# Kernel optimization log

Measured on AMD Instinct MI355X. Metric: run time of the kernel, lower is better.

## Reference

```python
import jax, jax.numpy as jnp
import numpy as np

DIM = 64   # model dim == d_inner (expand=1)
Hh = 64
Ww = 64
BATCH = 4
D_IN = 64
N_ST = 8   # d_state
DT_R = 4   # dt_rank = ceil(dim/16)
K = 4      # depthwise conv kernel
NB = 8     # total CrossMambaBlocks: 4 (depth=1) + 4 final cross blocks


def setup_inputs():
    key = jax.random.key(0)
    ks = iter(jax.random.split(key, 40))
    def rn(shape, s=0.02):
        return jax.random.normal(next(ks), shape, jnp.float32) * s
    A_init = jnp.log(jnp.tile(jnp.arange(1, N_ST + 1, dtype=jnp.float32), (NB, D_IN, 1)))
    return dict(
        img1=rn((BATCH, DIM, Hh, Ww), 1.0), img2=rn((BATCH, DIM, Hh, Ww), 1.0),
        img1_sum=rn((BATCH, DIM, Hh, Ww), 1.0), img2_sum=rn((BATCH, DIM, Hh, Ww), 1.0),
        norm0_w=jnp.ones((NB, DIM)), norm0_b=jnp.zeros((NB, DIM)),
        norm1_w=jnp.ones((NB, DIM)), norm1_b=jnp.zeros((NB, DIM)),
        in_w=rn((NB, 2 * D_IN, DIM)), in_b=jnp.zeros((NB, 2 * D_IN)),
        conv_w_f=rn((NB, D_IN, 1, K), 0.1), conv_b_f=jnp.zeros((NB, D_IN)),
        conv_w_b=rn((NB, D_IN, 1, K), 0.1), conv_b_b=jnp.zeros((NB, D_IN)),
        xproj_w_f=rn((NB, DT_R + 2 * N_ST, D_IN)), xproj_w_b=rn((NB, DT_R + 2 * N_ST, D_IN)),
        dtproj_w_f=rn((NB, D_IN, DT_R), 0.1), dtproj_b_f=jnp.zeros((NB, D_IN)),
        dtproj_w_b=rn((NB, D_IN, DT_R), 0.1), dtproj_b_b=jnp.zeros((NB, D_IN)),
        A_log_f=A_init, A_log_b=A_init,
        D_f=jnp.ones((NB, D_IN)), D_b=jnp.ones((NB, D_IN)),
        ln_w=jnp.ones((NB, D_IN)), ln_b=jnp.zeros((NB, D_IN)),
        mout_w=rn((NB, DIM, D_IN)), mout_b=jnp.zeros((NB, DIM)),
        fop_w=rn((DIM, 2 * DIM)), fop_b=jnp.zeros((DIM,)),
    )


def _ln(x, w, b):
    m = x.mean(-1, keepdims=True)
    v = ((x - m) ** 2).mean(-1, keepdims=True)
    return (x - m) * jax.lax.rsqrt(v + 1e-5) * w + b


def _dwconv(x, w, b):
    # x: [b,L,d], w: [d,1,K] depthwise causal conv along L
    y = jax.lax.conv_general_dilated(
        x.transpose(0, 2, 1), w, (1,), [(K - 1, 0)],
        dimension_numbers=('NCH', 'OIH', 'NCH'),
        feature_group_count=x.shape[-1])
    return y.transpose(0, 2, 1) + b


def _ssm(u, dt, Bm, Cm, A, Dm):
    # u,dt: [b,L,d]; Bm,Cm: [b,L,n]; A: [d,n]; Dm: [d]
    dA = jnp.exp(dt[..., None] * A)                 # [b,L,d,n]
    dBu = (dt * u)[..., None] * Bm[:, :, None, :]   # [b,L,d,n]
    def step(h, xs):
        dA_t, dBu_t, C_t = xs
        h = dA_t * h + dBu_t
        return h, jnp.einsum('bdn,bn->bd', h, C_t)
    h0 = jnp.zeros(u.shape[:1] + A.shape, u.dtype)
    _, ys = jax.lax.scan(step, h0, (jnp.moveaxis(dA, 1, 0), jnp.moveaxis(dBu, 1, 0), jnp.moveaxis(Cm, 1, 0)))
    return jnp.moveaxis(ys, 0, 1) + u * Dm


def _direction(x_in, extra, conv_w, conv_b, xproj_w, dtproj_w, dtproj_b, A_log, Dm, flip):
    if flip:
        x_in = x_in[:, ::-1]
        extra = extra[:, ::-1]
    u = jax.nn.silu(_dwconv(x_in, conv_w, conv_b))
    dbl = jnp.einsum('bld,ed->ble', extra, xproj_w)     # cross: dt/B/C from extra embedding
    dtr = dbl[..., :DT_R]
    Bm = dbl[..., DT_R:DT_R + N_ST]
    Cm = dbl[..., DT_R + N_ST:]
    dt = jax.nn.softplus(jnp.einsum('blr,dr->bld', dtr, dtproj_w) + dtproj_b)
    y = _ssm(u, dt, Bm, Cm, -jnp.exp(A_log), Dm)
    if flip:
        y = y[:, ::-1]
    return y


def _cross_block(i, x, extra, p):
    skip = x
    x = _ln(x, p['norm0_w'][i], p['norm0_b'][i])
    extra = _ln(extra, p['norm1_w'][i], p['norm1_b'][i])
    xz = jnp.einsum('bld,ed->ble', x, p['in_w'][i]) + p['in_b'][i]
    x_in, z = xz[..., :D_IN], xz[..., D_IN:]
    y_f = _direction(x_in, extra, p['conv_w_f'][i], p['conv_b_f'][i], p['xproj_w_f'][i],
                     p['dtproj_w_f'][i], p['dtproj_b_f'][i], p['A_log_f'][i], p['D_f'][i], False)
    y_b = _direction(x_in, extra, p['conv_w_b'][i], p['conv_b_b'][i], p['xproj_w_b'][i],
                     p['dtproj_w_b'][i], p['dtproj_b_b'][i], p['A_log_b'][i], p['D_b'][i], True)
    y = 0.5 * (y_f + y_b)                    # if_devide_out=True
    y = _ln(y, p['ln_w'][i], p['ln_b'][i])   # use_norm=True
    y = y * jax.nn.silu(z)
    out = jnp.einsum('bld,ed->ble', y, p['mout_w'][i]) + p['mout_b'][i]
    return out + skip


def _forward(img1, img2, img1_sum, img2_sum, norm0_w, norm0_b, norm1_w, norm1_b, in_w, in_b,
             conv_w_f, conv_b_f, conv_w_b, conv_b_b, xproj_w_f, xproj_w_b,
             dtproj_w_f, dtproj_b_f, dtproj_w_b, dtproj_b_b, A_log_f, A_log_b,
             D_f, D_b, ln_w, ln_b, mout_w, mout_b, fop_w, fop_b):
    p = dict(norm0_w=norm0_w, norm0_b=norm0_b, norm1_w=norm1_w, norm1_b=norm1_b,
             in_w=in_w, in_b=in_b, conv_w_f=conv_w_f, conv_b_f=conv_b_f,
             conv_w_b=conv_w_b, conv_b_b=conv_b_b, xproj_w_f=xproj_w_f, xproj_w_b=xproj_w_b,
             dtproj_w_f=dtproj_w_f, dtproj_b_f=dtproj_b_f, dtproj_w_b=dtproj_w_b,
             dtproj_b_b=dtproj_b_b, A_log_f=A_log_f, A_log_b=A_log_b, D_f=D_f, D_b=D_b,
             ln_w=ln_w, ln_b=ln_b, mout_w=mout_w, mout_b=mout_b)
    def seq(t):
        b, c, h, w = t.shape
        return t.reshape(b, c, h * w).transpose(0, 2, 1)   # b (h w) c
    s1, s2, s1s, s2s = seq(img1), seq(img2), seq(img1_sum), seq(img2_sum)
    # depth=1 cross-fusion loop
    s1 = _cross_block(0, s1, s1s, p)
    s2 = _cross_block(1, s2, s2s, p)
    s1s = _cross_block(2, s1s, s1, p)
    s2s = _cross_block(3, s2s, s2, p)
    # final cross blocks
    i1l = _cross_block(4, s1, s2, p)
    i1g = _cross_block(5, s1, s2s, p)
    i2l = _cross_block(6, s2, s1, p)
    i2g = _cross_block(7, s2, s1s, p)
    c1 = jnp.concatenate([i1l, i1g], -1)
    c2 = jnp.concatenate([i2l, i2g], -1)
    fusion = jnp.einsum('ble,ce->blc', 0.5 * (c1 + c2), fop_w) + fop_b
    b = img1.shape[0]
    return fusion.transpose(0, 2, 1).reshape(b, DIM, Hh, Ww)


def reference(img1, img2, img1_sum, img2_sum, norm0_w, norm0_b, norm1_w, norm1_b, in_w, in_b,
              conv_w_f, conv_b_f, conv_w_b, conv_b_b, xproj_w_f, xproj_w_b,
              dtproj_w_f, dtproj_b_f, dtproj_w_b, dtproj_b_b, A_log_f, A_log_b,
              D_f, D_b, ln_w, ln_b, mout_w, mout_b, fop_w, fop_b):
    return _forward(img1, img2, img1_sum, img2_sum, norm0_w, norm0_b, norm1_w, norm1_b, in_w, in_b,
                    conv_w_f, conv_b_f, conv_w_b, conv_b_b, xproj_w_f, xproj_w_b,
                    dtproj_w_f, dtproj_b_f, dtproj_w_b, dtproj_b_b, A_log_f, A_log_b,
                    D_f, D_b, ln_w, ln_b, mout_w, mout_b, fop_w, fop_b)
```

## Files before the change

### kernel.cpp

```cpp
#include <hip/hip_runtime.h>
#include <hip/hip_bf16.h>

#define BX 4
#define LX 4096
#define DX 64
#define NX 8
#define TCH 16
#define NCH 256
#define BLD (BX*LX*DX)

typedef unsigned short u16;
typedef __attribute__((ext_vector_type(8))) short v8s;
typedef __attribute__((ext_vector_type(4))) float v4f;

#define L2E 1.44269504088896f
#define LN2 0.69314718055994531f

__device__ __forceinline__ float b2f(u16 u){ return __uint_as_float(((unsigned)u)<<16); }
__device__ __forceinline__ u16 f2b(float f){
  unsigned u = __float_as_uint(f);
  unsigned r = (u + 0x7FFFu + ((u>>16)&1u)) >> 16;
  return (u16)r;
}
__device__ __forceinline__ float siluf(float x){
  return x * __builtin_amdgcn_rcpf(1.f + __builtin_amdgcn_exp2f(-x*L2E));
}
__device__ __forceinline__ float softplusf(float x){
  const float t = __builtin_amdgcn_exp2f(-fabsf(x)*L2E);
  return fmaxf(x, 0.f) + LN2 * __builtin_amdgcn_logf(1.f + t);
}

__device__ __forceinline__ v4f mfma16(v8s a, v8s b, v4f c){
  return __builtin_amdgcn_mfma_f32_16x16x32_bf16(a, b, c, 0, 0, 0);
}
__device__ __forceinline__ void split8(const float* v, v8s& hi, v8s& lo){
  #pragma unroll
  for(int j=0;j<8;j++){
    const short h = (short)f2b(v[j]);
    hi[j] = h;
    lo[j] = (short)f2b(v[j] - b2f((u16)h));
  }
}
__device__ __forceinline__ void afrag(const float* tile, int lane, int k0, v8s& hi, v8s& lo){
  const float* p = tile + (lane&15)*72 + k0 + ((lane>>4)<<3);
  float v[8];
  const float4 a = *(const float4*)(p);
  const float4 b = *(const float4*)(p+4);
  v[0]=a.x; v[1]=a.y; v[2]=a.z; v[3]=a.w;
  v[4]=b.x; v[5]=b.y; v[6]=b.z; v[7]=b.w;
  split8(v, hi, lo);
}

struct Ctx {
  const float *nw0,*nb0,*nw1,*nb1;
  const float *inb;
  const float *convw,*convb;
  const float *dtw,*dtb;
  const float *A2,*Dp;
  const float *lnw,*lnb;
  const float *moutb;
  const float *fopb;
  const u16 *wih,*wil,*wxh,*wxl,*wmh,*wml,*wfh,*wfl;
  float *act[4], *outc[4];
  float *xin[4], *zz[4], *dbl[4], *yy[4], *Pp[4], *qq[4], *hin[4];
};

struct BlkDesc { int i; const float* x; const float* e; float* out; int slot; };
struct StageArgs { BlkDesc d[4]; };

struct PrepEnt { const void* src; float* dst; int n; int mode; };
struct PrepAll { PrepEnt a[21]; };
struct WPrep { const void* sA; const void* sB; u16* dh; u16* dl; long off; int E; int KS; int kind; int i; };
struct WPrepAll { WPrep a[25]; };

__global__ __launch_bounds__(256) void k_prep(PrepAll pa, WPrepAll wa, const u16* df){
  const bool isbf = (df[0] == 0x3F80u);
  if(blockIdx.y < 21){
    PrepEnt p = pa.a[blockIdx.y];
    int idx = blockIdx.x*256 + threadIdx.x;
    if(idx < p.n){
      float v = isbf ? b2f(((const u16*)p.src)[idx]) : ((const float*)p.src)[idx];
      if(p.mode==2) v = -__expf(v) * L2E;
      p.dst[idx] = v;
    }
  } else {
    WPrep p = wa.a[blockIdx.y - 21];
    const int wv = threadIdx.x >> 6, lane = threadIdx.x & 63;
    const int idx = blockIdx.x*4 + wv;
    const int NT = (p.E + 15) >> 4;
    if(idx >= NT*p.KS) return;
    const int ct = idx / p.KS, ks = idx % p.KS;
    const int g  = ct*16 + (lane & 15);
    const int k0 = ks*32 + ((lane>>4)<<3);
    const int K  = p.KS*32;
    bool valid; long si = 0; const void* sp = p.sA;
    if(p.kind == 1){
      valid = (g < 40);
      const int dir = g/20, e = g - dir*20;
      if(dir) sp = p.sB;
      si = ((long)p.i*20 + e)*64 + k0;
    } else {
      valid = (g < p.E);
      si = p.off + (long)g*K + k0;
    }
    float v[8];
    #pragma unroll
    for(int j2=0;j2<8;j2++){
      float x = 0.f;
      if(valid) x = isbf ? b2f(((const u16*)sp)[si+j2]) : ((const float*)sp)[si+j2];
      v[j2] = x;
    }
    v8s hi, lo; split8(v, hi, lo);
    const size_t o = ((size_t)idx*64 + lane)*8;
    *(v8s*)(p.dh + o) = hi;
    *(v8s*)(p.dl + o) = lo;
  }
}

struct SeqArgs { const void* src[4]; };

__global__ __launch_bounds__(256) void k_seq(SeqArgs s, Ctx c, const u16* df){
  const bool isbf = (df[0] == 0x3F80u);
  __shared__ float ld[64*65];
  const int t = blockIdx.z, b = blockIdx.y, l0 = blockIdx.x*64;
  float* dst = c.act[t];
  const int tx = threadIdx.x, ty = threadIdx.y;
  if(isbf){
    const u16* src = (const u16*)s.src[t];
    #pragma unroll
    for(int k=0;k<16;k++){ int d = k*4+ty; ld[d*65+tx] = b2f(src[(size_t)(b*64+d)*LX + l0+tx]); }
  } else {
    const float* src = (const float*)s.src[t];
    #pragma unroll
    for(int k=0;k<16;k++){ int d = k*4+ty; ld[d*65+tx] = src[(size_t)(b*64+d)*LX + l0+tx]; }
  }
  __syncthreads();
  #pragma unroll
  for(int k=0;k<16;k++){ int p = k*4+ty; dst[(size_t)(b*LX + l0+p)*64 + tx] = ld[tx*65+p]; }
}

__device__ __forceinline__ void coop72(float* sb, const float* g, int t){
  #pragma unroll
  for(int k=0;k<4;k++){
    const int idx = k*256 + t;
    const int row = idx >> 4;
    const int c4  = (idx & 15) << 2;
    *(float4*)(sb + row*72 + c4) = *(const float4*)(g + (size_t)row*64 + c4);
  }
}
__device__ __forceinline__ void coop72_avg(float* sb, const float* g0, const float* g1, int t){
  #pragma unroll
  for(int k=0;k<4;k++){
    const int idx = k*256 + t;
    const int row = idx >> 4;
    const int c4  = (idx & 15) << 2;
    const float4 a = *(const float4*)(g0 + (size_t)row*64 + c4);
    const float4 b = *(const float4*)(g1 + (size_t)row*64 + c4);
    float4 o; o.x=0.5f*(a.x+b.x); o.y=0.5f*(a.y+b.y); o.z=0.5f*(a.z+b.z); o.w=0.5f*(a.w+b.w);
    *(float4*)(sb + row*72 + c4) = o;
  }
}

__device__ __forceinline__ void ln72(float* sb, int lane, const float* w, const float* b){
  float r[64];
  float* p = sb + lane*72;
  #pragma unroll
  for(int cc=0;cc<64;cc+=4){ float4 v = *(const float4*)(p+cc); r[cc]=v.x; r[cc+1]=v.y; r[cc+2]=v.z; r[cc+3]=v.w; }
  float m=0.f;
  #pragma unroll
  for(int d=0;d<64;d++) m += r[d];
  m *= (1.f/64.f);
  float va=0.f;
  #pragma unroll
  for(int d=0;d<64;d++){ float t=r[d]-m; va += t*t; }
  va *= (1.f/64.f);
  const float rs = rsqrtf(va + 1e-5f);
  #pragma unroll
  for(int d=0;d<64;d++) r[d] = (r[d]-m)*rs*w[d] + b[d];
  #pragma unroll
  for(int cc=0;cc<64;cc+=4){ float4 v={r[cc],r[cc+1],r[cc+2],r[cc+3]}; *(float4*)(p+cc)=v; }
}

__global__ __launch_bounds__(256) void k_front(Ctx c, StageArgs sa){
  __shared__ __align__(16) float sx[64*72];
  __shared__ __align__(16) float se[64*72];
  const BlkDesc bd = sa.d[blockIdx.y];
  const int i = bd.i;
  const int tile = blockIdx.x;
  const int b = tile >> 6;
  const int l0 = (tile & 63) << 6;
  const int bl0 = b*LX + l0;
  const int t = threadIdx.x;
  const int wave = t >> 6, lane = t & 63;

  coop72(sx, bd.x + (size_t)bl0*64, t);
  coop72(se, bd.e + (size_t)bl0*64, t);
  __syncthreads();
  if(wave == 0)      ln72(sx, lane, c.nw0 + i*64, c.nb0 + i*64);
  else if(wave == 1) ln72(se, lane, c.nw1 + i*64, c.nb1 + i*64);
  __syncthreads();

  const int m0 = wave*16;
  const int q  = lane >> 4;
  const int n15 = lane & 15;

  {
    v8s ah[2], al[2];
    afrag(sx + m0*72, lane, 0,  ah[0], al[0]);
    afrag(sx + m0*72, lane, 32, ah[1], al[1]);
    const v8s* WH = (const v8s*)c.wih + (size_t)i*1024;
    const v8s* WL = (const v8s*)c.wil + (size_t)i*1024;
    #pragma unroll 1
    for(int ct=0; ct<8; ct++){
      const int colg = ct*16 + n15;
      const float bias = c.inb[i*128 + colg];
      v4f acc = {bias, bias, bias, bias};
      #pragma unroll
      for(int ks=0; ks<2; ks++){
        const v8s wh = WH[(ct*2+ks)*64 + lane];
        const v8s wl = WL[(ct*2+ks)*64 + lane];
        acc = mfma16(ah[ks], wl, acc);
        acc = mfma16(al[ks], wh, acc);
        acc = mfma16(ah[ks], wh, acc);
      }
      float* baseo = (colg < 64) ? c.xin[bd.slot] : c.zz[bd.slot];
      const int col = colg & 63;
      #pragma unroll
      for(int r=0;r<4;r++){
        const int row = m0 + q*4 + r;
        baseo[(size_t)(bl0+row)*64 + col] = acc[r];
      }
    }
  }
  {
    v8s ah[2], al[2];
    afrag(se + m0*72, lane, 0,  ah[0], al[0]);
    afrag(se + m0*72, lane, 32, ah[1], al[1]);
    const v8s* WH = (const v8s*)c.wxh + (size_t)i*384;
    const v8s* WL = (const v8s*)c.wxl + (size_t)i*384;
    #pragma unroll 1
    for(int ct=0; ct<3; ct++){
      v4f acc = {0.f,0.f,0.f,0.f};
      #pragma unroll
      for(int ks=0; ks<2; ks++){
        const v8s wh = WH[(ct*2+ks)*64 + lane];
        const v8s wl = WL[(ct*2+ks)*64 + lane];
        acc = mfma16(ah[ks], wl, acc);
        acc = mfma16(al[ks], wh, acc);
        acc = mfma16(ah[ks], wh, acc);
      }
      const int g = ct*16 + n15;
      if(g < 40){
        const int dir = (g >= 20);
        const int e = g - dir*20;
        float* dp = c.dbl[bd.slot] + (size_t)dir*((size_t)BX*LX*20);
        #pragma unroll
        for(int r=0;r<4;r++){
          const int row = m0 + q*4 + r;
          dp[(size_t)(bl0+row)*20 + e] = acc[r];
        }
      }
    }
  }
}

template<int PASS>
__device__ __forceinline__ void scan_body(const Ctx& c, const StageArgs& sa){
  __shared__ __align__(16) float meta[TCH*20];
  const int zid = blockIdx.z;
  const int j = zid >> 1, dir = zid & 1;
  const BlkDesc bd = sa.d[j];
  const int i = bd.i, slot = bd.slot;
  const int ch = blockIdx.x, b = blockIdx.y;
  const int d = threadIdx.x;
  const int pb = (dir*8 + i)*64 + d;

  const float4 cwv = *(const float4*)(c.convw + (size_t)pb*4);
  const float  cbv = c.convb[pb];
  const float4 dwv = *(const float4*)(c.dtw + (size_t)pb*4);
  const float  dtbv = c.dtb[pb];
  const float4 A2a = *(const float4*)(c.A2 + (size_t)pb*8);
  const float4 A2b = *(const float4*)(c.A2 + (size_t)pb*8 + 4);
  float A2[8] = {A2a.x,A2a.y,A2a.z,A2a.w,A2b.x,A2b.y,A2b.z,A2b.w};

  {
    const float4* s = (const float4*)(c.dbl[slot] + (size_t)dir*((size_t)BX*LX*20)
                                      + (size_t)(b*LX + ch*TCH)*20);
    float4* dst = (float4*)meta;
    #pragma unroll
    for(int k=0;k<2;k++){ int idx = k*64 + d; if(idx < 80) dst[idx] = s[idx]; }
  }
  __syncthreads();

  const float* X = c.xin[slot] + (size_t)b*LX*64 + d;
  float h[8];
  if(PASS==1){
    #pragma unroll
    for(int n=0;n<8;n++) h[n]=0.f;
  } else {
    const float* hp = c.hin[slot] + (size_t)(dir*NCH + ch)*((size_t)BX*512) + (size_t)b*512 + d;
    #pragma unroll
    for(int n=0;n<8;n++) h[n] = hp[n*64];
  }
  const float Dv = (PASS==3) ? c.Dp[pb] : 0.f;
  float* Y = (PASS==3) ? (c.yy[slot] + (size_t)(dir*BX + b)*LX*64 + d) : (float*)0;

  int lbase, sgn;
  if(dir==0){ lbase = ch*TCH;          sgn =  1; }
  else      { lbase = ch*TCH + TCH-1;  sgn = -1; }
  float w0,w1,w2;
  { int p0 = lbase - 3*sgn; w0 = (p0>=0 && p0<LX)? X[(size_t)p0*64] : 0.f; }
  { int p1 = lbase - 2*sgn; w1 = (p1>=0 && p1<LX)? X[(size_t)p1*64] : 0.f; }
  { int p2 = lbase - 1*sgn; w2 = (p2>=0 && p2<LX)? X[(size_t)p2*64] : 0.f; }

  const float* Xp = X + (size_t)lbase*64;
  float* Yp = (PASS==3) ? (Y + (size_t)lbase*64) : (float*)0;
  const float* mp = meta + (dir ? (TCH-1)*20 : 0);
  const int xstep = sgn*64;
  const int mstep = sgn*20;

  float S = 0.f;
  #pragma unroll 4
  for(int t=0;t<TCH;t++){
    const float xc = *Xp;
    const float u = siluf(cwv.x*w0 + cwv.y*w1 + cwv.z*w2 + cwv.w*xc + cbv);
    const float4 m0  = *(const float4*)(mp);
    const float4 mb0 = *(const float4*)(mp+4);
    const float4 mb1 = *(const float4*)(mp+8);
    const float dt = softplusf(m0.x*dwv.x + m0.y*dwv.y + m0.z*dwv.z + m0.w*dwv.w + dtbv);
    const float du = dt*u;
    const float Bv[8] = {mb0.x,mb0.y,mb0.z,mb0.w,mb1.x,mb1.y,mb1.z,mb1.w};
    #pragma unroll
    for(int n=0;n<8;n++){
      const float dA = __builtin_amdgcn_exp2f(dt*A2[n]);
      h[n] = dA*h[n] + du*Bv[n];
    }
    if(PASS==3){
      const float4 mc0 = *(const float4*)(mp+12);
      const float4 mc1 = *(const float4*)(mp+16);
      const float Cv[8] = {mc0.x,mc0.y,mc0.z,mc0.w,mc1.x,mc1.y,mc1.z,mc1.w};
      float yv = u*Dv;
      #pragma unroll
      for(int n=0;n<8;n++) yv += h[n]*Cv[n];
      *Yp = yv;
      Yp += xstep;
    } else {
      S += dt;
    }
    w0=w1; w1=w2; w2=xc;
    Xp += xstep; mp += mstep;
  }
  if(PASS==1){
    float* Pw = c.Pp[slot] + (size_t)(dir*NCH + ch)*((size_t)BX*512) + (size_t)b*512 + d;
    float* Qw = c.qq[slot] + (size_t)(dir*NCH + ch)*((size_t)BX*512) + (size_t)b*512 + d;
    #pragma unroll
    for(int n=0;n<8;n++){
      Pw[n*64] = __builtin_amdgcn_exp2f(A2[n]*S);
      Qw[n*64] = h[n];
    }
  }
}

__global__ __launch_bounds__(64) void k_scan1(Ctx c, StageArgs sa){ scan_body<1>(c, sa); }
__global__ __launch_bounds__(64) void k_scan3(Ctx c, StageArgs sa){ scan_body<3>(c, sa); }

__global__ __launch_bounds__(64) void k_mid(Ctx c, StageArgs sa){
  const int b = blockIdx.x >> 3;
  const int seg = blockIdx.x & 7;
  const int dir = blockIdx.y & 1, j = blockIdx.y >> 1;
  const BlkDesc bd = sa.d[j];
  const int slot = bd.slot;
  const int nd = seg*64 + threadIdx.x;
  const size_t base = (size_t)dir*NCH*((size_t)BX*512) + (size_t)b*512 + nd;
  const size_t STR = (size_t)BX*512;
  const float* P = c.Pp[slot] + base;
  const float* Q = c.qq[slot] + base;
  float* H = c.hin[slot] + base;
  float h = 0.f;
  float Pv[32], Qv[32];
  #pragma unroll 1
  for(int g=0; g<NCH/32; g++){
    #pragma unroll
    for(int k=0;k<32;k++){
      const int ch = dir ? (NCH-1 - (g*32+k)) : (g*32+k);
      Pv[k] = P[(size_t)ch*STR]; Qv[k] = Q[(size_t)ch*STR];
    }
    #pragma unroll
    for(int k=0;k<32;k++){
      const int ch = dir ? (NCH-1 - (g*32+k)) : (g*32+k);
      H[(size_t)ch*STR] = h;
      h = fmaf(Pv[k], h, Qv[k]);
    }
  }
}

__global__ __launch_bounds__(256) void k_back(Ctx c, StageArgs sa){
  __shared__ __align__(16) float sy[64*72];
  __shared__ __align__(16) float sz[64*72];
  __shared__ __align__(16) float sk[64*72];
  const BlkDesc bd = sa.d[blockIdx.y];
  const int i = bd.i, slot = bd.slot;
  const int tile = blockIdx.x;
  const int b = tile >> 6;
  const int l0 = (tile & 63) << 6;
  const int bl0 = b*LX + l0;
  const int t = threadIdx.x;
  const int wave = t >> 6, lane = t & 63;

  coop72_avg(sy, c.yy[slot] + (size_t)b*LX*64 + (size_t)l0*64,
                 c.yy[slot] + (size_t)(BX+b)*LX*64 + (size_t)l0*64, t);
  coop72(sz, c.zz[slot] + (size_t)bl0*64, t);
  coop72(sk, bd.x + (size_t)bl0*64, t);
  __syncthreads();
  if(wave == 0){
    ln72(sy, lane, c.lnw + i*64, c.lnb + i*64);
    float* p = sy + lane*72;
    const float* zp = sz + lane*72;
    #pragma unroll
    for(int d=0;d<64;d++){ p[d] *= siluf(zp[d]); }
  }
  __syncthreads();

  const int m0 = wave*16;
  const int q  = lane >> 4;
  const int n15 = lane & 15;
  v8s ah[2], al[2];
  afrag(sy + m0*72, lane, 0,  ah[0], al[0]);
  afrag(sy + m0*72, lane, 32, ah[1], al[1]);
  const v8s* WH = (const v8s*)c.wmh + (size_t)i*512;
  const v8s* WL = (const v8s*)c.wml + (size_t)i*512;
  #pragma unroll 1
  for(int ct=0; ct<4; ct++){
    const int col = ct*16 + n15;
    const float bias = c.moutb[i*64 + col];
    v4f acc = {bias, bias, bias, bias};
    #pragma unroll
    for(int ks=0; ks<2; ks++){
      const v8s wh = WH[(ct*2+ks)*64 + lane];
      const v8s wl = WL[(ct*2+ks)*64 + lane];
      acc = mfma16(ah[ks], wl, acc);
      acc = mfma16(al[ks], wh, acc);
      acc = mfma16(ah[ks], wh, acc);
    }
    #pragma unroll
    for(int r=0;r<4;r++){
      const int row = m0 + q*4 + r;
      bd.out[(size_t)(bl0+row)*64 + col] = acc[r] + sk[row*72 + col];
    }
  }
}

__global__ __launch_bounds__(256) void k_fusion(Ctx c, void* outp, const u16* df){
  const bool isbf = (df[0] == 0x3F80u);
  __shared__ __align__(16) float sL[64*72];
  __shared__ __align__(16) float sH[64*72];
  __shared__ __align__(16) float sT[64*68];
  const int tile = blockIdx.x;
  const int b = tile >> 6;
  const int l0 = (tile & 63) << 6;
  const int bl0 = b*LX + l0;
  const int t = threadIdx.x;
  const int wave = t >> 6, lane = t & 63;

  coop72_avg(sL, c.outc[0] + (size_t)bl0*64, c.outc[2] + (size_t)bl0*64, t);
  coop72_avg(sH, c.outc[1] + (size_t)bl0*64, c.outc[3] + (size_t)bl0*64, t);
  __syncthreads();

  const int m0 = wave*16;
  const int q  = lane >> 4;
  const int n15 = lane & 15;
  v8s ah[4], al[4];
  afrag(sL + m0*72, lane, 0,  ah[0], al[0]);
  afrag(sL + m0*72, lane, 32, ah[1], al[1]);
  afrag(sH + m0*72, lane, 0,  ah[2], al[2]);
  afrag(sH + m0*72, lane, 32, ah[3], al[3]);
  const v8s* WH = (const v8s*)c.wfh;
  const v8s* WL = (const v8s*)c.wfl;
  #pragma unroll 1
  for(int ct=0; ct<4; ct++){
    const int col = ct*16 + n15;
    const float bias = c.fopb[col];
    v4f acc = {bias, bias, bias, bias};
    #pragma unroll
    for(int ks=0; ks<4; ks++){
      const v8s wh = WH[(ct*4+ks)*64 + lane];
      const v8s wl = WL[(ct*4+ks)*64 + lane];
      acc = mfma16(ah[ks], wl, acc);
      acc = mfma16(al[ks], wh, acc);
      acc = mfma16(ah[ks], wh, acc);
    }
    #pragma unroll
    for(int r=0;r<4;r++) sT[col*68 + m0 + q*4 + r] = acc[r];
  }
  __syncthreads();

  const int o  = t >> 2;
  const int p0 = (t & 3) * 16;
  float v[16];
  #pragma unroll
  for(int k=0;k<16;k+=4){
    const float4 x = *(const float4*)(sT + o*68 + p0 + k);
    v[k]=x.x; v[k+1]=x.y; v[k+2]=x.z; v[k+3]=x.w;
  }
  const size_t off = (size_t)(b*64+o)*LX + l0 + p0;
  if(isbf){
    u16 hb[16];
    #pragma unroll
    for(int k=0;k<16;k++) hb[k] = f2b(v[k]);
    uint4 u0, u1;
    u0.x = hb[0] | ((unsigned)hb[1]<<16);  u0.y = hb[2] | ((unsigned)hb[3]<<16);
    u0.z = hb[4] | ((unsigned)hb[5]<<16);  u0.w = hb[6] | ((unsigned)hb[7]<<16);
    u1.x = hb[8] | ((unsigned)hb[9]<<16);  u1.y = hb[10]| ((unsigned)hb[11]<<16);
    u1.z = hb[12]| ((unsigned)hb[13]<<16); u1.w = hb[14]| ((unsigned)hb[15]<<16);
    *(uint4*)((u16*)outp + off)     = u0;
    *(uint4*)((u16*)outp + off + 8) = u1;
  } else {
    float* fo = (float*)outp + off;
    #pragma unroll
    for(int k=0;k<16;k+=4){ float4 x={v[k],v[k+1],v[k+2],v[k+3]}; *(float4*)(fo+k)=x; }
  }
}

extern "C" void kernel_launch(void* const* d_in, const int* in_sizes, int n_in,
                              void* d_out, int out_size, void* d_ws, size_t ws_size,
                              hipStream_t stream){
  (void)in_sizes; (void)out_size;
  if(n_in < 30) return;
  const u16* df = (const u16*)d_in[22];
  float* w = (float*)d_ws;
  size_t off = 0;
  auto al = [&](size_t n){ float* p = w + off; off += n; return p; };

  Ctx c;
  float* nw0 = al(512);  float* nb0 = al(512);
  float* nw1 = al(512);  float* nb1 = al(512);
  float* inb = al(1024);
  float* convw = al(4096); float* convb = al(1024);
  float* dtw = al(4096); float* dtb = al(1024);
  float* A2 = al(8192);  float* Dp = al(1024);
  float* lnw = al(512);  float* lnb = al(512);
  float* moutb = al(512);
  float* fopb = al(64);
  c.nw0=nw0; c.nb0=nb0; c.nw1=nw1; c.nb1=nb1;
  c.inb=inb; c.convw=convw; c.convb=convb;
  c.dtw=dtw; c.dtb=dtb; c.A2=A2; c.Dp=Dp;
  c.lnw=lnw; c.lnb=lnb; c.moutb=moutb; c.fopb=fopb;

  u16* wih = (u16*)al(32768); u16* wil = (u16*)al(32768);
  u16* wxh = (u16*)al(12288); u16* wxl = (u16*)al(12288);
  u16* wmh = (u16*)al(16384); u16* wml = (u16*)al(16384);
  u16* wfh = (u16*)al(4096);  u16* wfl = (u16*)al(4096);
  c.wih=wih; c.wil=wil; c.wxh=wxh; c.wxl=wxl; c.wmh=wmh; c.wml=wml; c.wfh=wfh; c.wfl=wfl;

  for(int k=0;k<4;k++) c.act[k]  = al(BLD);
  for(int k=0;k<4;k++) c.outc[k] = al(BLD);

  const size_t CHW = 2*(size_t)NCH*BX*512;
  const size_t SLOT = (size_t)BLD + BLD + 2*(size_t)BX*LX*20 + 2*(size_t)BLD + 3*CHW;
  const size_t avail = ws_size/4;
  int nslots = 4;
  while(nslots>1 && off + (size_t)nslots*SLOT > avail) nslots >>= 1;
  for(int s=0;s<nslots;s++){
    c.xin[s]=al(BLD); c.zz[s]=al(BLD); c.dbl[s]=al(2*(size_t)BX*LX*20);
    c.yy[s]=al(2*(size_t)BLD);
    c.Pp[s]=al(CHW); c.qq[s]=al(CHW); c.hin[s]=al(CHW);
  }
  for(int s=nslots;s<4;s++){
    c.xin[s]=c.xin[0]; c.zz[s]=c.zz[0]; c.dbl[s]=c.dbl[0]; c.yy[s]=c.yy[0];
    c.Pp[s]=c.Pp[0]; c.qq[s]=c.qq[0]; c.hin[s]=c.hin[0];
  }

  PrepAll pa;
  int kk = 0;
  auto add = [&](int idx, float* dst, int n, int mode){
    pa.a[kk].src=d_in[idx]; pa.a[kk].dst=dst; pa.a[kk].n=n; pa.a[kk].mode=mode; kk++;
  };
  add(4,  nw0, 512, 0); add(5,  nb0, 512, 0);
  add(6,  nw1, 512, 0); add(7,  nb1, 512, 0);
  add(9,  inb, 1024, 0);
  add(10, convw, 2048, 0);      add(11, convb, 512, 0);
  add(12, convw+2048, 2048, 0); add(13, convb+512, 512, 0);
  add(16, dtw, 2048, 0);        add(17, dtb, 512, 0);
  add(18, dtw+2048, 2048, 0);   add(19, dtb+512, 512, 0);
  add(20, A2, 4096, 2);         add(21, A2+4096, 4096, 2);
  add(22, Dp, 512, 0);          add(23, Dp+512, 512, 0);
  add(24, lnw, 512, 0);         add(25, lnb, 512, 0);
  add(27, moutb, 512, 0);
  add(29, fopb, 64, 0);

  WPrepAll wa;
  for(int i=0;i<8;i++) wa.a[i]    = { d_in[8],  nullptr,  wih+(size_t)i*8192, wil+(size_t)i*8192, (long)i*8192, 128, 2, 0, i };
  for(int i=0;i<8;i++) wa.a[8+i]  = { d_in[14], d_in[15], wxh+(size_t)i*3072, wxl+(size_t)i*3072, 0,            48, 2, 1, i };
  for(int i=0;i<8;i++) wa.a[16+i] = { d_in[26], nullptr,  wmh+(size_t)i*4096, wml+(size_t)i*4096, (long)i*4096, 64, 2, 0, i };
  wa.a[24] = { d_in[28], nullptr, wfh, wfl, 0, 64, 4, 0, 0 };

  k_prep<<<dim3(16,46),256,0,stream>>>(pa, wa, df);

  SeqArgs sq;
  for(int t=0;t<4;t++) sq.src[t] = d_in[t];
  k_seq<<<dim3(64,BX,4), dim3(64,4), 0, stream>>>(sq, c, df);

  BlkDesc R1[2] = {{0, c.act[0], c.act[2], c.act[0], 0},
                   {1, c.act[1], c.act[3], c.act[1], 0}};
  BlkDesc R2[4] = {{2, c.act[2], c.act[0], c.act[2], 0},
                   {3, c.act[3], c.act[1], c.act[3], 0},
                   {4, c.act[0], c.act[1], c.outc[0], 0},
                   {6, c.act[1], c.act[0], c.outc[2], 0}};
  BlkDesc R3[2] = {{5, c.act[0], c.act[3], c.outc[1], 0},
                   {7, c.act[1], c.act[2], c.outc[3], 0}};

  auto run = [&](BlkDesc* ds, int cnt){
    for(int k=0;k<cnt;k+=nslots){
      int n = cnt-k; if(n>nslots) n = nslots;
      StageArgs sa;
      for(int j=0;j<n;j++){ sa.d[j] = ds[k+j]; sa.d[j].slot = j; }
      for(int j=n;j<4;j++) sa.d[j] = sa.d[0];
      k_front<<<dim3(256,n),      256, 0, stream>>>(c, sa);
      k_scan1<<<dim3(NCH,BX,2*n),  64, 0, stream>>>(c, sa);
      k_mid  <<<dim3(BX*8,2*n),    64, 0, stream>>>(c, sa);
      k_scan3<<<dim3(NCH,BX,2*n),  64, 0, stream>>>(c, sa);
      k_back <<<dim3(256,n),      256, 0, stream>>>(c, sa);
    }
  };
  run(R1,2); run(R2,4); run(R3,2);
  k_fusion<<<256,256,0,stream>>>(c, d_out, df);
}
```

Baseline: 376.5 us.

## Fuse chunk scan passes into front and back kernels, drop yy buffer

Folds the first scan pass (chunk-local state and decay products) into k_front. It reuses the in-projection outputs and x_proj metadata already held in shared memory, and recomputes a 3-row conv halo on each side of the tile with a scalar LN plus projection. The second scan pass moves into k_back, which averages both directions straight into shared memory. That removes the yy global buffer and two kernel launches per stage. The cost is redundant halo recomputation, more register pressure from the 22-element x windows and unrolled loops, and fewer waves running scans than the separate kernels had.

```diff
diff --git a/kernel.cpp b/kernel.cpp
--- a/kernel.cpp
+++ b/kernel.cpp
@@ -60,31 +60,40 @@
   const float *lnw,*lnb;
   const float *moutb;
   const float *fopb;
+  const float *inwxT;
   const u16 *wih,*wil,*wxh,*wxl,*wmh,*wml,*wfh,*wfl;
   float *act[4], *outc[4];
-  float *xin[4], *zz[4], *dbl[4], *yy[4], *Pp[4], *qq[4], *hin[4];
+  float *xin[4], *zz[4], *dbl[4], *Pp[4], *qq[4], *hin[4];
 };
 
 struct BlkDesc { int i; const float* x; const float* e; float* out; int slot; };
 struct StageArgs { BlkDesc d[4]; };
 
-struct PrepEnt { const void* src; float* dst; int n; int mode; };
-struct PrepAll { PrepEnt a[21]; };
+struct PrepEnt { const void* src; float* dst; int n; int mode; long soff; };
+struct PrepAll { PrepEnt a[29]; };
 struct WPrep { const void* sA; const void* sB; u16* dh; u16* dl; long off; int E; int KS; int kind; int i; };
 struct WPrepAll { WPrep a[25]; };
 
 __global__ __launch_bounds__(256) void k_prep(PrepAll pa, WPrepAll wa, const u16* df){
   const bool isbf = (df[0] == 0x3F80u);
-  if(blockIdx.y < 21){
+  if(blockIdx.y < 29){
     PrepEnt p = pa.a[blockIdx.y];
     int idx = blockIdx.x*256 + threadIdx.x;
     if(idx < p.n){
-      float v = isbf ? b2f(((const u16*)p.src)[idx]) : ((const float*)p.src)[idx];
-      if(p.mode==2) v = -__expf(v) * L2E;
+      float v;
+      if(p.mode == 3){
+        const int cc = idx & 63, dd = idx >> 6;
+        const long si = p.soff + (long)cc*64 + dd;
+        v = isbf ? b2f(((const u16*)p.src)[si]) : ((const float*)p.src)[si];
+      } else {
+        const long si = p.soff + idx;
+        v = isbf ? b2f(((const u16*)p.src)[si]) : ((const float*)p.src)[si];
+        if(p.mode==2) v = -__expf(v) * L2E;
+      }
       p.dst[idx] = v;
     }
   } else {
-    WPrep p = wa.a[blockIdx.y - 21];
+    WPrep p = wa.a[blockIdx.y - 29];
     const int wv = threadIdx.x >> 6, lane = threadIdx.x & 63;
     const int idx = blockIdx.x*4 + wv;
     const int NT = (p.E + 15) >> 4;
@@ -204,10 +213,41 @@
   const int q  = lane >> 4;
   const int n15 = lane & 15;
 
+  v8s xah[2], xal[2], eah[2], eal[2];
+  afrag(sx + m0*72, lane, 0,  xah[0], xal[0]);
+  afrag(sx + m0*72, lane, 32, xah[1], xal[1]);
+  afrag(se + m0*72, lane, 0,  eah[0], eal[0]);
+  afrag(se + m0*72, lane, 32, eah[1], eal[1]);
+  __syncthreads();
+
+  float* sxin  = sx;
+  float* shalo = se;
+  float* smeta = se + 512;
+  float* shx   = se + 3072;
+  float* svalid= se + 3456;
+
+  if(wave < 3){
+    #pragma unroll
+    for(int pp=0;pp<2;pp++){
+      const int hr = pp*3 + wave;
+      const int r = (hr<3) ? (l0 - 3 + hr) : (l0 + 64 + (hr-3));
+      const bool ok = (r >= 0 && r < LX);
+      float xv = ok ? bd.x[(size_t)(b*LX + r)*64 + lane] : 0.f;
+      float s = xv;
+      #pragma unroll
+      for(int o=32;o>0;o>>=1) s += __shfl_xor(s,o);
+      const float m = s*(1.f/64.f);
+      const float dv = xv - m;
+      float v2 = dv*dv;
+      #pragma unroll
+      for(int o=32;o>0;o>>=1) v2 += __shfl_xor(v2,o);
+      const float rs = rsqrtf(v2*(1.f/64.f) + 1e-5f);
+      shx[hr*64+lane] = ok ? (dv*rs*c.nw0[i*64+lane] + c.nb0[i*64+lane]) : 0.f;
+      if(lane==0) svalid[hr] = ok ? 1.f : 0.f;
+    }
+  }
+
   {
-    v8s ah[2], al[2];
-    afrag(sx + m0*72, lane, 0,  ah[0], al[0]);
-    afrag(sx + m0*72, lane, 32, ah[1], al[1]);
     const v8s* WH = (const v8s*)c.wih + (size_t)i*1024;
     const v8s* WL = (const v8s*)c.wil + (size_t)i*1024;
     #pragma unroll 1
@@ -219,23 +259,29 @@
       for(int ks=0; ks<2; ks++){
         const v8s wh = WH[(ct*2+ks)*64 + lane];
         const v8s wl = WL[(ct*2+ks)*64 + lane];
-        acc = mfma16(ah[ks], wl, acc);
-        acc = mfma16(al[ks], wh, acc);
-        acc = mfma16(ah[ks], wh, acc);
-      }
-      float* baseo = (colg < 64) ? c.xin[bd.slot] : c.zz[bd.slot];
-      const int col = colg & 63;
-      #pragma unroll
-      for(int r=0;r<4;r++){
-        const int row = m0 + q*4 + r;
-        baseo[(size_t)(bl0+row)*64 + col] = acc[r];
+        acc = mfma16(xah[ks], wl, acc);
+        acc = mfma16(xal[ks], wh, acc);
+        acc = mfma16(xah[ks], wh, acc);
+      }
+      if(colg < 64){
+        float* gx = c.xin[bd.slot];
+        #pragma unroll
+        for(int r=0;r<4;r++){
+          const int row = m0 + q*4 + r;
+          gx[(size_t)(bl0+row)*64 + colg] = acc[r];
+          sxin[row*72 + colg] = acc[r];
+        }
+      } else {
+        const int col = colg - 64;
+        #pragma unroll
+        for(int r=0;r<4;r++){
+          const int row = m0 + q*4 + r;
+          c.zz[bd.slot][(size_t)(bl0+row)*64 + col] = acc[r];
+        }
       }
     }
   }
   {
-    v8s ah[2], al[2];
-    afrag(se + m0*72, lane, 0,  ah[0], al[0]);
-    afrag(se + m0*72, lane, 32, ah[1], al[1]);
     const v8s* WH = (const v8s*)c.wxh + (size_t)i*384;
     const v8s* WL = (const v8s*)c.wxl + (size_t)i*384;
     #pragma unroll 1
@@ -245,9 +291,9 @@
       for(int ks=0; ks<2; ks++){
         const v8s wh = WH[(ct*2+ks)*64 + lane];
         const v8s wl = WL[(ct*2+ks)*64 + lane];
-        acc = mfma16(ah[ks], wl, acc);
-        acc = mfma16(al[ks], wh, acc);
-        acc = mfma16(ah[ks], wh, acc);
+        acc = mfma16(eah[ks], wl, acc);
+        acc = mfma16(eal[ks], wh, acc);
+        acc = mfma16(eah[ks], wh, acc);
       }
       const int g = ct*16 + n15;
       if(g < 40){
@@ -258,111 +304,90 @@
         for(int r=0;r<4;r++){
           const int row = m0 + q*4 + r;
           dp[(size_t)(bl0+row)*20 + e] = acc[r];
+          smeta[row*40 + g] = acc[r];
         }
       }
     }
   }
-}
-
-template<int PASS>
-__device__ __forceinline__ void scan_body(const Ctx& c, const StageArgs& sa){
-  __shared__ __align__(16) float meta[TCH*20];
-  const int zid = blockIdx.z;
-  const int j = zid >> 1, dir = zid & 1;
-  const BlkDesc bd = sa.d[j];
-  const int i = bd.i, slot = bd.slot;
-  const int ch = blockIdx.x, b = blockIdx.y;
-  const int d = threadIdx.x;
-  const int pb = (dir*8 + i)*64 + d;
-
-  const float4 cwv = *(const float4*)(c.convw + (size_t)pb*4);
-  const float  cbv = c.convb[pb];
-  const float4 dwv = *(const float4*)(c.dtw + (size_t)pb*4);
-  const float  dtbv = c.dtb[pb];
-  const float4 A2a = *(const float4*)(c.A2 + (size_t)pb*8);
-  const float4 A2b = *(const float4*)(c.A2 + (size_t)pb*8 + 4);
-  float A2[8] = {A2a.x,A2a.y,A2a.z,A2a.w,A2b.x,A2b.y,A2b.z,A2b.w};
+  __syncthreads();
+
+  #pragma unroll
+  for(int k=0;k<2;k++){
+    const int idx = k*256 + t;
+    if(idx < 384){
+      const int hr = idx >> 6, cc = idx & 63;
+      float a = 0.f;
+      if(svalid[hr] > 0.5f){
+        a = c.inb[i*128 + cc];
+        const float* wt = c.inwxT + (size_t)i*4096 + cc;
+        const float* sr = shx + hr*64;
+        #pragma unroll 4
+        for(int dd=0; dd<64; dd++) a += sr[dd]*wt[dd*64];
+      }
+      shalo[hr*64 + cc] = a;
+    }
+  }
+  __syncthreads();
 
   {
-    const float4* s = (const float4*)(c.dbl[slot] + (size_t)dir*((size_t)BX*LX*20)
-                                      + (size_t)(b*LX + ch*TCH)*20);
-    float4* dst = (float4*)meta;
-    #pragma unroll
-    for(int k=0;k<2;k++){ int idx = k*64 + d; if(idx < 80) dst[idx] = s[idx]; }
-  }
-  __syncthreads();
-
-  const float* X = c.xin[slot] + (size_t)b*LX*64 + d;
-  float h[8];
-  if(PASS==1){
-    #pragma unroll
-    for(int n=0;n<8;n++) h[n]=0.f;
-  } else {
-    const float* hp = c.hin[slot] + (size_t)(dir*NCH + ch)*((size_t)BX*512) + (size_t)b*512 + d;
-    #pragma unroll
-    for(int n=0;n<8;n++) h[n] = hp[n*64];
-  }
-  const float Dv = (PASS==3) ? c.Dp[pb] : 0.f;
-  float* Y = (PASS==3) ? (c.yy[slot] + (size_t)(dir*BX + b)*LX*64 + d) : (float*)0;
-
-  int lbase, sgn;
-  if(dir==0){ lbase = ch*TCH;          sgn =  1; }
-  else      { lbase = ch*TCH + TCH-1;  sgn = -1; }
-  float w0,w1,w2;
-  { int p0 = lbase - 3*sgn; w0 = (p0>=0 && p0<LX)? X[(size_t)p0*64] : 0.f; }
-  { int p1 = lbase - 2*sgn; w1 = (p1>=0 && p1<LX)? X[(size_t)p1*64] : 0.f; }
-  { int p2 = lbase - 1*sgn; w2 = (p2>=0 && p2<LX)? X[(size_t)p2*64] : 0.f; }
-
-  const float* Xp = X + (size_t)lbase*64;
-  float* Yp = (PASS==3) ? (Y + (size_t)lbase*64) : (float*)0;
-  const float* mp = meta + (dir ? (TCH-1)*20 : 0);
-  const int xstep = sgn*64;
-  const int mstep = sgn*20;
-
-  float S = 0.f;
-  #pragma unroll 4
-  for(int t=0;t<TCH;t++){
-    const float xc = *Xp;
-    const float u = siluf(cwv.x*w0 + cwv.y*w1 + cwv.z*w2 + cwv.w*xc + cbv);
-    const float4 m0  = *(const float4*)(mp);
-    const float4 mb0 = *(const float4*)(mp+4);
-    const float4 mb1 = *(const float4*)(mp+8);
-    const float dt = softplusf(m0.x*dwv.x + m0.y*dwv.y + m0.z*dwv.z + m0.w*dwv.w + dtbv);
-    const float du = dt*u;
-    const float Bv[8] = {mb0.x,mb0.y,mb0.z,mb0.w,mb1.x,mb1.y,mb1.z,mb1.w};
-    #pragma unroll
-    for(int n=0;n<8;n++){
-      const float dA = __builtin_amdgcn_exp2f(dt*A2[n]);
-      h[n] = dA*h[n] + du*Bv[n];
-    }
-    if(PASS==3){
-      const float4 mc0 = *(const float4*)(mp+12);
-      const float4 mc1 = *(const float4*)(mp+16);
-      const float Cv[8] = {mc0.x,mc0.y,mc0.z,mc0.w,mc1.x,mc1.y,mc1.z,mc1.w};
-      float yv = u*Dv;
-      #pragma unroll
-      for(int n=0;n<8;n++) yv += h[n]*Cv[n];
-      *Yp = yv;
-      Yp += xstep;
-    } else {
-      S += dt;
-    }
-    w0=w1; w1=w2; w2=xc;
-    Xp += xstep; mp += mstep;
-  }
-  if(PASS==1){
-    float* Pw = c.Pp[slot] + (size_t)(dir*NCH + ch)*((size_t)BX*512) + (size_t)b*512 + d;
-    float* Qw = c.qq[slot] + (size_t)(dir*NCH + ch)*((size_t)BX*512) + (size_t)b*512 + d;
-    #pragma unroll
-    for(int n=0;n<8;n++){
-      Pw[n*64] = __builtin_amdgcn_exp2f(A2[n]*S);
-      Qw[n*64] = h[n];
-    }
-  }
-}
-
-__global__ __launch_bounds__(64) void k_scan1(Ctx c, StageArgs sa){ scan_body<1>(c, sa); }
-__global__ __launch_bounds__(64) void k_scan3(Ctx c, StageArgs sa){ scan_body<3>(c, sa); }
+    const int ch = (tile & 63)*4 + wave;
+    const int d2 = lane;
+    float xs[22];
+    #pragma unroll
+    for(int k=0;k<22;k++){
+      const int r = m0 + k - 3;
+      float xv;
+      if(r < 0)        xv = shalo[(r+3)*64 + d2];
+      else if(r >= 64) xv = shalo[(r-61)*64 + d2];
+      else             xv = sxin[r*72 + d2];
+      xs[k] = xv;
+    }
+    #pragma unroll
+    for(int dir=0; dir<2; dir++){
+      const int pb = (dir*8 + i)*64 + d2;
+      const float4 cwv = *(const float4*)(c.convw + (size_t)pb*4);
+      const float  cbv = c.convb[pb];
+      const float4 dwv = *(const float4*)(c.dtw + (size_t)pb*4);
+      const float  dtbv = c.dtb[pb];
+      const float4 A2a = *(const float4*)(c.A2 + (size_t)pb*8);
+      const float4 A2b = *(const float4*)(c.A2 + (size_t)pb*8 + 4);
+      const float A2r[8] = {A2a.x,A2a.y,A2a.z,A2a.w,A2b.x,A2b.y,A2b.z,A2b.w};
+      float h[8];
+      #pragma unroll
+      for(int n=0;n<8;n++) h[n]=0.f;
+      float S=0.f;
+      #pragma unroll
+      for(int k=0;k<16;k++){
+        const int lr = dir ? (m0+15-k) : (m0+k);
+        const float w0 = dir ? xs[21-k] : xs[k];
+        const float w1 = dir ? xs[20-k] : xs[k+1];
+        const float w2 = dir ? xs[19-k] : xs[k+2];
+        const float xc = dir ? xs[18-k] : xs[k+3];
+        const float u = siluf(cwv.x*w0 + cwv.y*w1 + cwv.z*w2 + cwv.w*xc + cbv);
+        const float* m = smeta + lr*40 + dir*20;
+        const float4 m0v = *(const float4*)(m);
+        const float dt = softplusf(m0v.x*dwv.x + m0v.y*dwv.y + m0v.z*dwv.z + m0v.w*dwv.w + dtbv);
+        const float du = dt*u;
+        const float4 mb0 = *(const float4*)(m+4);
+        const float4 mb1 = *(const float4*)(m+8);
+        const float Bv[8] = {mb0.x,mb0.y,mb0.z,mb0.w,mb1.x,mb1.y,mb1.z,mb1.w};
+        #pragma unroll
+        for(int n=0;n<8;n++){
+          const float dA = __builtin_amdgcn_exp2f(dt*A2r[n]);
+          h[n] = dA*h[n] + du*Bv[n];
+        }
+        S += dt;
+      }
+      float* Pw = c.Pp[bd.slot] + (size_t)(dir*NCH + ch)*((size_t)BX*512) + (size_t)b*512 + d2;
+      float* Qw = c.qq[bd.slot] + (size_t)(dir*NCH + ch)*((size_t)BX*512) + (size_t)b*512 + d2;
+      #pragma unroll
+      for(int n=0;n<8;n++){
+        Pw[n*64] = __builtin_amdgcn_exp2f(A2r[n]*S);
+        Qw[n*64] = h[n];
+      }
+    }
+  }
+}
 
 __global__ __launch_bounds__(64) void k_mid(Ctx c, StageArgs sa){
   const int b = blockIdx.x >> 3;
@@ -397,7 +422,7 @@
 __global__ __launch_bounds__(256) void k_back(Ctx c, StageArgs sa){
   __shared__ __align__(16) float sy[64*72];
   __shared__ __align__(16) float sz[64*72];
-  __shared__ __align__(16) float sk[64*72];
+  __shared__ __align__(16) float smeta[64*40];
   const BlkDesc bd = sa.d[blockIdx.y];
   const int i = bd.i, slot = bd.slot;
   const int tile = blockIdx.x;
@@ -407,21 +432,88 @@
   const int t = threadIdx.x;
   const int wave = t >> 6, lane = t & 63;
 
-  coop72_avg(sy, c.yy[slot] + (size_t)b*LX*64 + (size_t)l0*64,
-                 c.yy[slot] + (size_t)(BX+b)*LX*64 + (size_t)l0*64, t);
   coop72(sz, c.zz[slot] + (size_t)bl0*64, t);
-  coop72(sk, bd.x + (size_t)bl0*64, t);
+  #pragma unroll
+  for(int d2=0; d2<2; d2++){
+    const float4* s = (const float4*)(c.dbl[slot] + (size_t)d2*((size_t)BX*LX*20) + (size_t)bl0*20);
+    #pragma unroll
+    for(int k=0;k<2;k++){
+      const int idx = k*256 + t;
+      if(idx < 320){
+        const int row = idx/5, e4 = idx - row*5;
+        *(float4*)(smeta + row*40 + d2*20 + e4*4) = s[idx];
+      }
+    }
+  }
+  __syncthreads();
+
+  const int m0 = wave*16;
+  {
+    const int ch = (tile & 63)*4 + wave;
+    const int d2 = lane;
+    const float* X = c.xin[slot] + (size_t)b*LX*64 + d2;
+    float xs[22];
+    #pragma unroll
+    for(int k=0;k<22;k++){
+      const int r = l0 + m0 + k - 3;
+      xs[k] = (r>=0 && r<LX) ? X[(size_t)r*64] : 0.f;
+    }
+    #pragma unroll
+    for(int dir=0; dir<2; dir++){
+      const int pb = (dir*8 + i)*64 + d2;
+      const float4 cwv = *(const float4*)(c.convw + (size_t)pb*4);
+      const float  cbv = c.convb[pb];
+      const float4 dwv = *(const float4*)(c.dtw + (size_t)pb*4);
+      const float  dtbv = c.dtb[pb];
+      const float4 A2a = *(const float4*)(c.A2 + (size_t)pb*8);
+      const float4 A2b = *(const float4*)(c.A2 + (size_t)pb*8 + 4);
+      const float A2r[8] = {A2a.x,A2a.y,A2a.z,A2a.w,A2b.x,A2b.y,A2b.z,A2b.w};
+      const float Dv = c.Dp[pb];
+      float h[8];
+      const float* hp = c.hin[slot] + (size_t)(dir*NCH + ch)*((size_t)BX*512) + (size_t)b*512 + d2;
+      #pragma unroll
+      for(int n=0;n<8;n++) h[n] = hp[n*64];
+      #pragma unroll
+      for(int k=0;k<16;k++){
+        const int lr = dir ? (m0+15-k) : (m0+k);
+        const float w0 = dir ? xs[21-k] : xs[k];
+        const float w1 = dir ? xs[20-k] : xs[k+1];
+        const float w2 = dir ? xs[19-k] : xs[k+2];
+        const float xc = dir ? xs[18-k] : xs[k+3];
+        const float u = siluf(cwv.x*w0 + cwv.y*w1 + cwv.z*w2 + cwv.w*xc + cbv);
+        const float* m = smeta + lr*40 + dir*20;
+        const float4 m0v = *(const float4*)(m);
+        const float dt = softplusf(m0v.x*dwv.x + m0v.y*dwv.y + m0v.z*dwv.z + m0v.w*dwv.w + dtbv);
+        const float du = dt*u;
+        const float4 mb0 = *(const float4*)(m+4);
+        const float4 mb1 = *(const float4*)(m+8);
+        const float Bv[8] = {mb0.x,mb0.y,mb0.z,mb0.w,mb1.x,mb1.y,mb1.z,mb1.w};
+        float yv = u*Dv;
+        #pragma unroll
+        for(int n=0;n<8;n++){
+          const float dA = __builtin_amdgcn_exp2f(dt*A2r[n]);
+          h[n] = dA*h[n] + du*Bv[n];
+        }
+        const float4 mc0 = *(const float4*)(m+12);
+        const float4 mc1 = *(const float4*)(m+16);
+        const float Cv[8] = {mc0.x,mc0.y,mc0.z,mc0.w,mc1.x,mc1.y,mc1.z,mc1.w};
+        #pragma unroll
+        for(int n=0;n<8;n++) yv += h[n]*Cv[n];
+        if(dir==0) sy[lr*72 + d2] = 0.5f*yv;
+        else       sy[lr*72 + d2] += 0.5f*yv;
+      }
+    }
+  }
   __syncthreads();
   if(wave == 0){
     ln72(sy, lane, c.lnw + i*64, c.lnb + i*64);
     float* p = sy + lane*72;
     const float* zp = sz + lane*72;
     #pragma unroll
-    for(int d=0;d<64;d++){ p[d] *= siluf(zp[d]); }
-  }
-  __syncthreads();
-
-  const int m0 = wave*16;
+    for(int d3=0;d3<64;d3++){ p[d3] *= siluf(zp[d3]); }
+  }
+  __syncthreads();
+
   const int q  = lane >> 4;
   const int n15 = lane & 15;
   v8s ah[2], al[2];
@@ -445,7 +537,7 @@
     #pragma unroll
     for(int r=0;r<4;r++){
       const int row = m0 + q*4 + r;
-      bd.out[(size_t)(bl0+row)*64 + col] = acc[r] + sk[row*72 + col];
+      bd.out[(size_t)(bl0+row)*64 + col] = acc[r] + bd.x[(size_t)(bl0+row)*64 + col];
     }
   }
 }
@@ -541,10 +633,11 @@
   float* lnw = al(512);  float* lnb = al(512);
   float* moutb = al(512);
   float* fopb = al(64);
+  float* inwxT = al(32768);
   c.nw0=nw0; c.nb0=nb0; c.nw1=nw1; c.nb1=nb1;
   c.inb=inb; c.convw=convw; c.convb=convb;
   c.dtw=dtw; c.dtb=dtb; c.A2=A2; c.Dp=Dp;
-  c.lnw=lnw; c.lnb=lnb; c.moutb=moutb; c.fopb=fopb;
+  c.lnw=lnw; c.lnb=lnb; c.moutb=moutb; c.fopb=fopb; c.inwxT=inwxT;
 
   u16* wih = (u16*)al(32768); u16* wil = (u16*)al(32768);
   u16* wxh = (u16*)al(12288); u16* wxl = (u16*)al(12288);
@@ -556,37 +649,37 @@
   for(int k=0;k<4;k++) c.outc[k] = al(BLD);
 
   const size_t CHW = 2*(size_t)NCH*BX*512;
-  const size_t SLOT = (size_t)BLD + BLD + 2*(size_t)BX*LX*20 + 2*(size_t)BLD + 3*CHW;
+  const size_t SLOT = (size_t)BLD + BLD + 2*(size_t)BX*LX*20 + 3*CHW;
   const size_t avail = ws_size/4;
   int nslots = 4;
   while(nslots>1 && off + (size_t)nslots*SLOT > avail) nslots >>= 1;
   for(int s=0;s<nslots;s++){
     c.xin[s]=al(BLD); c.zz[s]=al(BLD); c.dbl[s]=al(2*(size_t)BX*LX*20);
-    c.yy[s]=al(2*(size_t)BLD);
     c.Pp[s]=al(CHW); c.qq[s]=al(CHW); c.hin[s]=al(CHW);
   }
   for(int s=nslots;s<4;s++){
-    c.xin[s]=c.xin[0]; c.zz[s]=c.zz[0]; c.dbl[s]=c.dbl[0]; c.yy[s]=c.yy[0];
+    c.xin[s]=c.xin[0]; c.zz[s]=c.zz[0]; c.dbl[s]=c.dbl[0];
     c.Pp[s]=c.Pp[0]; c.qq[s]=c.qq[0]; c.hin[s]=c.hin[0];
   }
 
   PrepAll pa;
   int kk = 0;
-  auto add = [&](int idx, float* dst, int n, int mode){
-    pa.a[kk].src=d_in[idx]; pa.a[kk].dst=dst; pa.a[kk].n=n; pa.a[kk].mode=mode; kk++;
+  auto add = [&](int idx, float* dst, int n, int mode, long soff){
+    pa.a[kk].src=d_in[idx]; pa.a[kk].dst=dst; pa.a[kk].n=n; pa.a[kk].mode=mode; pa.a[kk].soff=soff; kk++;
   };
-  add(4,  nw0, 512, 0); add(5,  nb0, 512, 0);
-  add(6,  nw1, 512, 0); add(7,  nb1, 512, 0);
-  add(9,  inb, 1024, 0);
-  add(10, convw, 2048, 0);      add(11, convb, 512, 0);
-  add(12, convw+2048, 2048, 0); add(13, convb+512, 512, 0);
-  add(16, dtw, 2048, 0);        add(17, dtb, 512, 0);
-  add(18, dtw+2048, 2048, 0);   add(19, dtb+512, 512, 0);
-  add(20, A2, 4096, 2);         add(21, A2+4096, 4096, 2);
-  add(22, Dp, 512, 0);          add(23, Dp+512, 512, 0);
-  add(24, lnw, 512, 0);         add(25, lnb, 512, 0);
-  add(27, moutb, 512, 0);
-  add(29, fopb, 64, 0);
+  add(4,  nw0, 512, 0, 0); add(5,  nb0, 512, 0, 0);
+  add(6,  nw1, 512, 0, 0); add(7,  nb1, 512, 0, 0);
+  add(9,  inb, 1024, 0, 0);
+  add(10, convw, 2048, 0, 0);      add(11, convb, 512, 0, 0);
+  add(12, convw+2048, 2048, 0, 0); add(13, convb+512, 512, 0, 0);
+  add(16, dtw, 2048, 0, 0);        add(17, dtb, 512, 0, 0);
+  add(18, dtw+2048, 2048, 0, 0);   add(19, dtb+512, 512, 0, 0);
+  add(20, A2, 4096, 2, 0);         add(21, A2+4096, 4096, 2, 0);
+  add(22, Dp, 512, 0, 0);          add(23, Dp+512, 512, 0, 0);
+  add(24, lnw, 512, 0, 0);         add(25, lnb, 512, 0, 0);
+  add(27, moutb, 512, 0, 0);
+  add(29, fopb, 64, 0, 0);
+  for(int i=0;i<8;i++) add(8, inwxT + (size_t)i*4096, 4096, 3, (long)i*8192);
 
   WPrepAll wa;
   for(int i=0;i<8;i++) wa.a[i]    = { d_in[8],  nullptr,  wih+(size_t)i*8192, wil+(size_t)i*8192, (long)i*8192, 128, 2, 0, i };
@@ -594,7 +687,7 @@
   for(int i=0;i<8;i++) wa.a[16+i] = { d_in[26], nullptr,  wmh+(size_t)i*4096, wml+(size_t)i*4096, (long)i*4096, 64, 2, 0, i };
   wa.a[24] = { d_in[28], nullptr, wfh, wfl, 0, 64, 4, 0, 0 };
 
-  k_prep<<<dim3(16,46),256,0,stream>>>(pa, wa, df);
+  k_prep<<<dim3(16,54),256,0,stream>>>(pa, wa, df);
 
   SeqArgs sq;
   for(int t=0;t<4;t++) sq.src[t] = d_in[t];
@@ -615,11 +708,9 @@
       StageArgs sa;
       for(int j=0;j<n;j++){ sa.d[j] = ds[k+j]; sa.d[j].slot = j; }
       for(int j=n;j<4;j++) sa.d[j] = sa.d[0];
-      k_front<<<dim3(256,n),      256, 0, stream>>>(c, sa);
-      k_scan1<<<dim3(NCH,BX,2*n),  64, 0, stream>>>(c, sa);
-      k_mid  <<<dim3(BX*8,2*n),    64, 0, stream>>>(c, sa);
-      k_scan3<<<dim3(NCH,BX,2*n),  64, 0, stream>>>(c, sa);
-      k_back <<<dim3(256,n),      256, 0, stream>>>(c, sa);
+      k_front<<<dim3(256,n), 256, 0, stream>>>(c, sa);
+      k_mid  <<<dim3(BX*8,2*n), 64, 0, stream>>>(c, sa);
+      k_back <<<dim3(256,n), 256, 0, stream>>>(c, sa);
     }
   };
   run(R1,2); run(R2,4); run(R3,2);
```

Result: no change. 381.3 us (+1.3%).
